# Kernel optimization log

Hardware: AMD Instinct MI355X
Metric: run time of the kernel (lower is better)

Reference implementation:

```python
import jax, jax.numpy as jnp
import numpy as np

N_NODES = 1024
BATCH = 64
N = N_NODES * BATCH          # 65536 total nodes
BBX, LBL = 7, 1
H1, H2, H3 = 512, 16, 4096
LAT = 512
NCLS = 160
N_EDGES = 262144


def setup_inputs() -> dict:
    key = jax.random.key(0)
    ks = jax.random.split(key, 20)
    g = lambda k, shape: (jax.random.normal(k, shape, jnp.float32) * 0.02)
    inp = dict(
        E=jax.random.randint(ks[0], (2, N_EDGES), 0, N, dtype=jnp.int64),
        X_data=jax.random.normal(ks[1], (N, BBX + LBL), jnp.float32),
        class_labels=jax.random.uniform(ks[2], (BATCH * NCLS,), jnp.float32),
        # GCNConv weights (no bias, no normalize, no self-loops)
        W_g1=g(ks[3], (BBX + LBL, H1)),
        W_g2=g(ks[4], (H1, H2)),
        # dense layers ([in, out] convention; y = x @ W + b)
        W_box=g(ks[5], (BBX, H2)), b_box=jnp.zeros((H2,), jnp.float32),
        W_lbl=g(ks[6], (LBL, H2)), b_lbl=jnp.zeros((H2,), jnp.float32),
        W_d1=g(ks[7], (H2 * N_NODES, H3)), b_d1=jnp.zeros((H3,), jnp.float32),
        W_d2=g(ks[8], (H2 * N_NODES + NCLS, H3)), b_d2=jnp.zeros((H3,), jnp.float32),
        W_d3=g(ks[9], (H3, H3)), b_d3=jnp.zeros((H3,), jnp.float32),
        W_z=g(ks[10], (H3, LAT)), b_z=jnp.zeros((LAT,), jnp.float32),
    )
    return inp


def reference(E, X_data, class_labels, W_g1, W_g2, W_box, b_box, W_lbl, b_lbl,
              W_d1, b_d1, W_d2, b_d2, W_d3, b_d3, W_z, b_z):
    relu = jax.nn.relu
    src, dst = E[0], E[1]
    # GCNConv (normalize=False, add_self_loops=False, bias=False):
    # out[i] = sum_{(j->i) in E} (x @ W)[j]
    x = jax.ops.segment_sum((X_data @ W_g1)[src], dst, num_segments=N)   # [N, H1]
    x = jax.ops.segment_sum((x @ W_g2)[src], dst, num_segments=N)        # [N, H2]
    x = x.reshape(BATCH, N_NODES * H2)                                   # [B, 16*num_nodes]
    boxes = relu(X_data[:, 1:].reshape(BATCH, N_NODES, BBX) @ W_box + b_box)
    labels = relu(X_data[:, :1].reshape(BATCH, N_NODES, LBL) @ W_lbl + b_lbl)
    mix = (boxes + labels).reshape(BATCH, N_NODES * H2)
    mix = relu(mix @ W_d1 + b_d1)                                        # [B, H3]
    cls = class_labels.reshape(BATCH, NCLS)
    x = jnp.concatenate([cls, x], axis=-1)                               # [B, NCLS + 16*num_nodes]
    x = relu(x @ W_d2 + b_d2)
    x = x + mix
    x = relu(x @ W_d3 + b_d3)
    x = relu(x @ W_d3 + b_d3)
    z_mean = relu(x @ W_z + b_z)
    z_logvar = relu(x @ W_z + b_z)
    return (z_mean, z_logvar)
```

## Files before the change

### kernel.cpp

```cpp
#include <hip/hip_runtime.h>
#include <stdint.h>

typedef unsigned short u16;
typedef short bf16x8 __attribute__((ext_vector_type(8)));
typedef short bf16x4 __attribute__((ext_vector_type(4)));
typedef float f32x4 __attribute__((ext_vector_type(4)));

#define NTOT   65536
#define NB     64
#define NEDGE  262144
#define H3     4096
#define LATD   512
#define NCLS_  160
#define K1     16384
#define K2     16544

static __device__ __forceinline__ u16 f2b(float f) {
  uint32_t x = __float_as_uint(f);
  return (u16)((x + 0x7FFFu + ((x >> 16) & 1u)) >> 16);
}

__global__ void k_hist(const int* __restrict__ E, int* __restrict__ cnt,
                       const float* __restrict__ Wg1, const float* __restrict__ Wg2,
                       float* __restrict__ Wc) {
  int e = blockIdx.x * 256 + threadIdx.x;
  atomicAdd(&cnt[E[NEDGE + e]], 1);
  if (blockIdx.x == 0 && threadIdx.x < 128) {
    int c = threadIdx.x >> 4, h = threadIdx.x & 15;
    float acc = 0.f;
    for (int k = 0; k < 512; ++k) acc += Wg1[c * 512 + k] * Wg2[k * 16 + h];
    Wc[c * 16 + h] = acc;
  }
}

__global__ __launch_bounds__(1024) void k_scan(const int* __restrict__ cnt,
                                               int* __restrict__ off,
                                               int* __restrict__ cur) {
  __shared__ int wsum[16];
  const int t = threadIdx.x;
  const int lane = t & 63, w = t >> 6;
  const int base = t << 6;
  int s = 0;
  const int4* c4 = (const int4*)(cnt + base);
  #pragma unroll 4
  for (int i = 0; i < 16; ++i) { int4 v = c4[i]; s += v.x + v.y + v.z + v.w; }
  int sc = s;
  #pragma unroll
  for (int d = 1; d < 64; d <<= 1) {
    int u = __shfl_up(sc, d);
    if (lane >= d) sc += u;
  }
  if (lane == 63) wsum[w] = sc;
  __syncthreads();
  if (w == 0 && lane < 16) {
    int v = wsum[lane];
    #pragma unroll
    for (int d = 1; d < 16; d <<= 1) {
      int u = __shfl_up(v, d);
      if (lane >= d) v += u;
    }
    wsum[lane] = v;
  }
  __syncthreads();
  int run = (w == 0 ? 0 : wsum[w - 1]) + (sc - s);
  int4* o4 = (int4*)(off + base);
  int4* u4 = (int4*)(cur + base);
  #pragma unroll 4
  for (int i = 0; i < 16; ++i) {
    int4 v = c4[i];
    int4 r;
    r.x = run; run += v.x;
    r.y = run; run += v.y;
    r.z = run; run += v.z;
    r.w = run; run += v.w;
    o4[i] = r; u4[i] = r;
  }
}

__global__ void k_scatter(const int* __restrict__ E, int* __restrict__ cur,
                          int* __restrict__ csr) {
  int e = blockIdx.x * 256 + threadIdx.x;
  int p = atomicAdd(&cur[E[NEDGE + e]], 1);
  csr[p] = E[e];
}

__global__ void k_gather(const int* __restrict__ off, const int* __restrict__ cnt,
                         const int* __restrict__ csr, const float* __restrict__ In,
                         float* __restrict__ Out) {
  int t = blockIdx.x * 256 + threadIdx.x;
  int n = t >> 3, c = t & 7;
  int b = off[n], e = b + cnt[n];
  float acc = 0.f;
  for (int j = b; j < e; ++j) acc += In[(size_t)csr[j] * 8 + c];
  Out[(size_t)n * 8 + c] = acc;
}

__global__ void k_nodes(const float* __restrict__ S2, const float* __restrict__ Wc,
                        const float* __restrict__ X,
                        const float* __restrict__ Wbox, const float* __restrict__ bbox,
                        const float* __restrict__ Wlbl, const float* __restrict__ blbl,
                        const float* __restrict__ cls,
                        u16* __restrict__ Abuf, u16* __restrict__ Mbuf) {
  int idx = blockIdx.x * 256 + threadIdx.x;
  if (idx < NB * NCLS_) {
    int m = idx / NCLS_, i = idx - m * NCLS_;
    Abuf[(size_t)m * K2 + i] = f2b(cls[idx]);
  }
  if (idx >= NTOT * 16) return;
  int n = idx >> 4, h = idx & 15;
  int m = n >> 10, nl = n & 1023;
  const float* s2 = S2 + (size_t)n * 8;
  float xg = 0.f;
  #pragma unroll
  for (int c = 0; c < 8; ++c) xg += s2[c] * Wc[c * 16 + h];
  Abuf[(size_t)m * K2 + 160 + nl * 16 + h] = f2b(xg);
  const float* xr = X + (size_t)n * 8;
  float box = bbox[h];
  #pragma unroll
  for (int c = 0; c < 7; ++c) box += xr[1 + c] * Wbox[c * 16 + h];
  box = box > 0.f ? box : 0.f;
  float lb = xr[0] * Wlbl[h] + blbl[h];
  lb = lb > 0.f ? lb : 0.f;
  Mbuf[(size_t)m * K1 + nl * 16 + h] = f2b(box + lb);
}

#define CVTPK(dst, lo, hi) \
  asm("v_cvt_pk_bf16_f32 %0, %1, %2" : "=v"(dst) : "v"(lo), "v"(hi))

#define WPACK(I2, WwR)                                                         \
  { const int n_ = (l << 2) + (I2);                                            \
    const int sw_ = ((n_ >> 1) ^ (n_ >> 2)) & 3;                               \
    uint32_t q0, q1, q2, q3;                                                   \
    CVTPK(q0, ws0[I2], ws1[I2]);                                               \
    CVTPK(q1, ws2[I2], ws3[I2]);                                               \
    CVTPK(q2, ws4[I2], ws5[I2]);                                               \
    CVTPK(q3, ws6[I2], ws7[I2]);                                               \
    uint4 pk_ = {q0, q1, q2, q3};                                              \
    *(uint4*)(&WwR[n_ * 32 + ((wv ^ sw_) << 3)]) = pk_; }

#define WLOADS(II)                                                             \
  { const float* gw_ = gW + (size_t)(II) * stepW;                              \
    ws0 = *(const f32x4*)(gw_);                                                \
    ws1 = *(const f32x4*)(gw_ + Nw);                                           \
    ws2 = *(const f32x4*)(gw_ + 2 * Nw);                                       \
    ws3 = *(const f32x4*)(gw_ + 3 * Nw);                                       \
    ws4 = *(const f32x4*)(gw_ + 4 * Nw);                                       \
    ws5 = *(const f32x4*)(gw_ + 5 * Nw);                                       \
    ws6 = *(const f32x4*)(gw_ + 6 * Nw);                                       \
    ws7 = *(const f32x4*)(gw_ + 7 * Nw);                                       \
    aS  = *(const int4*)(gA + (size_t)(II) * 32); }

#define MFMA_BF16 __builtin_amdgcn_mfma_f32_16x16x32_bf16

#define GEMM_STEP(ST, ArD, WrD, AwR, WwR)                                      \
  {                                                                            \
    bf16x8 a0 = *(const bf16x8*)(&ArD[foA]);                                   \
    bf16x8 a1 = *(const bf16x8*)(&ArD[foA + 512]);                             \
    bf16x8 a2 = *(const bf16x8*)(&ArD[foA + 1024]);                            \
    bf16x8 a3 = *(const bf16x8*)(&ArD[foA + 1536]);                            \
    bf16x8 b0 = *(const bf16x8*)(&WrD[foB]);                                   \
    bf16x8 b1 = *(const bf16x8*)(&WrD[foB + 512]);                             \
    bf16x8 b2 = *(const bf16x8*)(&WrD[foB + 1024]);                            \
    bf16x8 b3 = *(const bf16x8*)(&WrD[foB + 1536]);                            \
    *(int4*)(&AwR[t * 8]) = aS;                                                \
    WPACK(0, WwR) WPACK(1, WwR) WPACK(2, WwR) WPACK(3, WwR)                    \
    { const int ii = (ST) + 2 < ns ? (ST) + 2 : ns - 1;                        \
      WLOADS(ii) }                                                             \
    acc00 = MFMA_BF16(a0, b0, acc00, 0, 0, 0);                                 \
    acc01 = MFMA_BF16(a0, b1, acc01, 0, 0, 0);                                 \
    acc02 = MFMA_BF16(a0, b2, acc02, 0, 0, 0);                                 \
    acc03 = MFMA_BF16(a0, b3, acc03, 0, 0, 0);                                 \
    acc10 = MFMA_BF16(a1, b0, acc10, 0, 0, 0);                                 \
    acc11 = MFMA_BF16(a1, b1, acc11, 0, 0, 0);                                 \
    acc12 = MFMA_BF16(a1, b2, acc12, 0, 0, 0);                                 \
    acc13 = MFMA_BF16(a1, b3, acc13, 0, 0, 0);                                 \
    acc20 = MFMA_BF16(a2, b0, acc20, 0, 0, 0);                                 \
    acc21 = MFMA_BF16(a2, b1, acc21, 0, 0, 0);                                 \
    acc22 = MFMA_BF16(a2, b2, acc22, 0, 0, 0);                                 \
    acc23 = MFMA_BF16(a2, b3, acc23, 0, 0, 0);                                 \
    acc30 = MFMA_BF16(a3, b0, acc30, 0, 0, 0);                                 \
    acc31 = MFMA_BF16(a3, b1, acc31, 0, 0, 0);                                 \
    acc32 = MFMA_BF16(a3, b2, acc32, 0, 0, 0);                                 \
    acc33 = MFMA_BF16(a3, b3, acc33, 0, 0, 0);                                 \
    asm volatile("s_waitcnt lgkmcnt(0)" ::: "memory");                         \
    __builtin_amdgcn_s_barrier();                                              \
    asm volatile("" ::: "memory");                                             \
  }

__global__ __launch_bounds__(256) void k_gemm(
    const u16* __restrict__ A0, const u16* __restrict__ A1, int lda0, int lda1,
    const float* __restrict__ W0, const float* __restrict__ W1, int Nw,
    int tot0, int tot1, int per0, int per1, int slabBase1,
    float* __restrict__ Cs)
{
  __shared__ u16 lA0[2048];
  __shared__ u16 lA1[2048];
  __shared__ u16 lW0[8192];
  __shared__ u16 lW1[8192];

  const u16* A; int lda; const float* W; int tot, per, slab;
  if (blockIdx.z == 0) { A = A0; lda = lda0; W = W0; tot = tot0; per = per0; slab = blockIdx.y; }
  else                 { A = A1; lda = lda1; W = W1; tot = tot1; per = per1; slab = slabBase1 + blockIdx.y; }

  const int n0  = blockIdx.x << 8;
  const int sp0 = blockIdx.y * per;
  int ns = tot - sp0; if (ns > per) ns = per;
  if (ns <= 0) return;
  const int t  = threadIdx.x;
  const int l  = t & 63;
  const int wv = t >> 6;

  const int rA  = t >> 2;
  const int cAg = (t & 3) ^ ((rA >> 1) & 3);
  const u16* gA = A + (size_t)rA * lda + cAg * 8 + (size_t)sp0 * 32;

  const float* gW = W + (size_t)(sp0 * 32 + wv * 8) * Nw + n0 + l * 4;
  const size_t stepW = (size_t)32 * Nw;

  const int g4 = l >> 4;
  const int li = l & 15;
  const int foA = li * 32 + ((g4 ^ ((li >> 1) & 3)) << 3);
  const int foB = wv * 2048 + li * 32 +
                  ((g4 ^ (((li >> 1) ^ (li >> 2)) & 3)) << 3);

  f32x4 z4 = {0.f, 0.f, 0.f, 0.f};
  f32x4 acc00 = z4, acc01 = z4, acc02 = z4, acc03 = z4;
  f32x4 acc10 = z4, acc11 = z4, acc12 = z4, acc13 = z4;
  f32x4 acc20 = z4, acc21 = z4, acc22 = z4, acc23 = z4;
  f32x4 acc30 = z4, acc31 = z4, acc32 = z4, acc33 = z4;

  f32x4 ws0, ws1, ws2, ws3, ws4, ws5, ws6, ws7;
  int4 aS;

  WLOADS(0)
  *(int4*)(&lA0[t * 8]) = aS;
  WPACK(0, lW0) WPACK(1, lW0) WPACK(2, lW0) WPACK(3, lW0)
  { const int i1 = 1 < ns ? 1 : 0;
    WLOADS(i1) }
  asm volatile("s_waitcnt lgkmcnt(0)" ::: "memory");
  __builtin_amdgcn_s_barrier();
  asm volatile("" ::: "memory");

  int st = 0;
  for (; st + 2 <= ns; st += 2) {
    GEMM_STEP(st,     lA0, lW0, lA1, lW1)
    GEMM_STEP(st + 1, lA1, lW1, lA0, lW0)
  }
  if (st < ns) {
    GEMM_STEP(st, lA0, lW0, lA1, lW1)
  }

  float* base = Cs + (size_t)slab * NB * Nw + n0 + wv * 64 + li;
  #pragma unroll
  for (int j = 0; j < 4; ++j) {
    float* r0 = base + (size_t)(g4 * 4 + j) * Nw;
    r0[0]                    = acc00[j];
    r0[16]                   = acc01[j];
    r0[32]                   = acc02[j];
    r0[48]                   = acc03[j];
    float* r1 = r0 + 16 * Nw;
    r1[0]                    = acc10[j];
    r1[16]                   = acc11[j];
    r1[32]                   = acc12[j];
    r1[48]                   = acc13[j];
    float* r2 = r0 + 32 * Nw;
    r2[0]                    = acc20[j];
    r2[16]                   = acc21[j];
    r2[32]                   = acc22[j];
    r2[48]                   = acc23[j];
    float* r3 = r0 + 48 * Nw;
    r3[0]                    = acc30[j];
    r3[16]                   = acc31[j];
    r3[32]                   = acc32[j];
    r3[48]                   = acc33[j];
  }
}

__global__ void k_ep12(const float* __restrict__ Cs,
                       const float* __restrict__ b1, const float* __restrict__ b2,
                       u16* __restrict__ A3) {
  int i = blockIdx.x * 256 + threadIdx.x;
  if (i >= NB * H3) return;
  float mix = b1[i & (H3 - 1)];
  float v   = b2[i & (H3 - 1)];
  #pragma unroll 4
  for (int s = 0; s < 16; ++s)  mix += Cs[(size_t)s * (NB * H3) + i];
  #pragma unroll 4
  for (int s = 16; s < 32; ++s) v   += Cs[(size_t)s * (NB * H3) + i];
  mix = mix > 0.f ? mix : 0.f;
  v   = v   > 0.f ? v   : 0.f;
  A3[i] = f2b(v + mix);
}

__global__ void k_ep(const float* __restrict__ Cs, int nslab, int slabElems,
                     const float* __restrict__ bias, u16* __restrict__ outb,
                     int colmask, int total) {
  int i = blockIdx.x * 256 + threadIdx.x;
  if (i >= total) return;
  float v = bias[i & colmask];
  #pragma unroll 4
  for (int s = 0; s < nslab; ++s) v += Cs[(size_t)s * slabElems + i];
  v = v > 0.f ? v : 0.f;
  outb[i] = f2b(v);
}

__global__ void k_ep5(const float* __restrict__ Cs, int nslab,
                      const float* __restrict__ bz, float* __restrict__ out) {
  int i = blockIdx.x * 256 + threadIdx.x;
  if (i >= NB * LATD) return;
  float v = bz[i & 511];
  #pragma unroll 4
  for (int s = 0; s < nslab; ++s) v += Cs[(size_t)s * (NB * LATD) + i];
  v = v > 0.f ? v : 0.f;
  out[i] = v;
  out[NB * LATD + i] = v;
}

extern "C" void kernel_launch(void* const* d_in, const int* in_sizes, int n_in,
                              void* d_out, int out_size, void* d_ws, size_t ws_size,
                              hipStream_t stream) {
  const int*   E    = (const int*)d_in[0];
  const float* X    = (const float*)d_in[1];
  const float* cls  = (const float*)d_in[2];
  const float* Wg1  = (const float*)d_in[3];
  const float* Wg2  = (const float*)d_in[4];
  const float* Wbox = (const float*)d_in[5];
  const float* bbox = (const float*)d_in[6];
  const float* Wlbl = (const float*)d_in[7];
  const float* blbl = (const float*)d_in[8];
  const float* Wd1  = (const float*)d_in[9];
  const float* bd1  = (const float*)d_in[10];
  const float* Wd2  = (const float*)d_in[11];
  const float* bd2  = (const float*)d_in[12];
  const float* Wd3  = (const float*)d_in[13];
  const float* bd3  = (const float*)d_in[14];
  const float* Wz   = (const float*)d_in[15];
  const float* bz   = (const float*)d_in[16];

  char* ws = (char*)d_ws;
  int*   cnt  = (int*)  (ws + 0x000000);
  int*   off  = (int*)  (ws + 0x040000);
  int*   cur  = (int*)  (ws + 0x080000);
  int*   csr  = (int*)  (ws + 0x0C0000);
  float* S1   = (float*)(ws + 0x1C0000);
  float* S2   = (float*)(ws + 0x3C0000);
  float* Wc   = (float*)(ws + 0x5C0000);
  u16*   A3   = (u16*)  (ws + 0x5C1000);
  u16*   A4   = (u16*)  (ws + 0x641000);
  u16*   A5   = (u16*)  (ws + 0x6C1000);
  u16*   Mbuf = (u16*)  (ws + 0x741000);
  u16*   Abuf = (u16*)  (ws + 0x941000);
  float* Cslb = (float*)(ws + 0xB50000);

  hipMemsetAsync(cnt, 0, 0x40000, stream);
  k_hist   <<<NEDGE / 256, 256, 0, stream>>>(E, cnt, Wg1, Wg2, Wc);
  k_scan   <<<1, 1024, 0, stream>>>(cnt, off, cur);
  k_scatter<<<NEDGE / 256, 256, 0, stream>>>(E, cur, csr);
  k_gather <<<NTOT * 8 / 256, 256, 0, stream>>>(off, cnt, csr, X,  S1);
  k_gather <<<NTOT * 8 / 256, 256, 0, stream>>>(off, cnt, csr, S1, S2);
  k_nodes  <<<NTOT * 16 / 256, 256, 0, stream>>>(S2, Wc, X, Wbox, bbox, Wlbl, blbl,
                                                 cls, Abuf, Mbuf);

  { dim3 g(16, 16, 2);
    k_gemm<<<g, 256, 0, stream>>>(Mbuf, Abuf, K1, K2, Wd1, Wd2, H3,
                                  512, 517, 32, 33, 16, Cslb); }
  k_ep12<<<NB * H3 / 256, 256, 0, stream>>>(Cslb, bd1, bd2, A3);

  { dim3 g(16, 16, 1);
    k_gemm<<<g, 256, 0, stream>>>(A3, A3, H3, H3, Wd3, Wd3, H3,
                                  128, 128, 8, 8, 0, Cslb); }
  k_ep<<<NB * H3 / 256, 256, 0, stream>>>(Cslb, 16, NB * H3, bd3, A4, H3 - 1, NB * H3);

  { dim3 g(16, 16, 1);
    k_gemm<<<g, 256, 0, stream>>>(A4, A4, H3, H3, Wd3, Wd3, H3,
                                  128, 128, 8, 8, 0, Cslb); }
  k_ep<<<NB * H3 / 256, 256, 0, stream>>>(Cslb, 16, NB * H3, bd3, A5, H3 - 1, NB * H3);

  { dim3 g(2, 32, 1);
    k_gemm<<<g, 256, 0, stream>>>(A5, A5, H3, H3, Wz, Wz, LATD,
                                  128, 128, 4, 4, 0, Cslb); }
  k_ep5<<<NB * LATD / 256, 256, 0, stream>>>(Cslb, 32, bz, (float*)d_out);
}
```

Measured before the change: 296.7 us.

## Make GEMM weight tiles wave-private, load A to registers, double split-K

Each wave of the GEMM now stages only its own 64-column slice of the weight tile in LDS. This removes the block-wide barrier at every K step. The A operand is loaded straight from global memory into registers, one step ahead, instead of going through shared memory. Split-K slabs are doubled (grid y 16→32, per-slab steps halved) to put more blocks in flight on the bandwidth-bound weight stream, and launch bounds now ask for 3 blocks per CU. In exchange, each wave issues redundant A global loads and more fp32 partial-sum slabs are written and then reduced in the epilogues.

```diff
diff --git a/kernel.cpp b/kernel.cpp
--- a/kernel.cpp
+++ b/kernel.cpp
@@ -127,16 +127,7 @@
 #define CVTPK(dst, lo, hi) \
   asm("v_cvt_pk_bf16_f32 %0, %1, %2" : "=v"(dst) : "v"(lo), "v"(hi))
 
-#define WPACK(I2, WwR)                                                         \
-  { const int n_ = (l << 2) + (I2);                                            \
-    const int sw_ = ((n_ >> 1) ^ (n_ >> 2)) & 3;                               \
-    uint32_t q0, q1, q2, q3;                                                   \
-    CVTPK(q0, ws0[I2], ws1[I2]);                                               \
-    CVTPK(q1, ws2[I2], ws3[I2]);                                               \
-    CVTPK(q2, ws4[I2], ws5[I2]);                                               \
-    CVTPK(q3, ws6[I2], ws7[I2]);                                               \
-    uint4 pk_ = {q0, q1, q2, q3};                                              \
-    *(uint4*)(&WwR[n_ * 32 + ((wv ^ sw_) << 3)]) = pk_; }
+#define MFMA_BF16 __builtin_amdgcn_mfma_f32_16x16x32_bf16
 
 #define WLOADS(II)                                                             \
   { const float* gw_ = gW + (size_t)(II) * stepW;                              \
@@ -147,25 +138,33 @@
     ws4 = *(const f32x4*)(gw_ + 4 * Nw);                                       \
     ws5 = *(const f32x4*)(gw_ + 5 * Nw);                                       \
     ws6 = *(const f32x4*)(gw_ + 6 * Nw);                                       \
-    ws7 = *(const f32x4*)(gw_ + 7 * Nw);                                       \
-    aS  = *(const int4*)(gA + (size_t)(II) * 32); }
-
-#define MFMA_BF16 __builtin_amdgcn_mfma_f32_16x16x32_bf16
-
-#define GEMM_STEP(ST, ArD, WrD, AwR, WwR)                                      \
+    ws7 = *(const f32x4*)(gw_ + 7 * Nw); }
+
+#define ALOADS(II)                                                             \
+  { const u16* ga_ = gA + (size_t)(II) * 32;                                   \
+    a0 = *(const bf16x8*)(ga_);                                                \
+    a1 = *(const bf16x8*)(ga_ + rtA);                                          \
+    a2 = *(const bf16x8*)(ga_ + 2 * rtA);                                      \
+    a3 = *(const bf16x8*)(ga_ + 3 * rtA); }
+
+#define WPACK(I2, Lw)                                                          \
+  { uint32_t q0, q1, q2, q3;                                                   \
+    CVTPK(q0, ws0[I2], ws1[I2]);                                               \
+    CVTPK(q1, ws2[I2], ws3[I2]);                                               \
+    CVTPK(q2, ws4[I2], ws5[I2]);                                               \
+    CVTPK(q3, ws6[I2], ws7[I2]);                                               \
+    uint4 pk_ = {q0, q1, q2, q3};                                              \
+    *(uint4*)(&Lw[wo##I2]) = pk_; }
+
+#define GEMM_STEP(ST, Lr, Lw)                                                  \
   {                                                                            \
-    bf16x8 a0 = *(const bf16x8*)(&ArD[foA]);                                   \
-    bf16x8 a1 = *(const bf16x8*)(&ArD[foA + 512]);                             \
-    bf16x8 a2 = *(const bf16x8*)(&ArD[foA + 1024]);                            \
-    bf16x8 a3 = *(const bf16x8*)(&ArD[foA + 1536]);                            \
-    bf16x8 b0 = *(const bf16x8*)(&WrD[foB]);                                   \
-    bf16x8 b1 = *(const bf16x8*)(&WrD[foB + 512]);                             \
-    bf16x8 b2 = *(const bf16x8*)(&WrD[foB + 1024]);                            \
-    bf16x8 b3 = *(const bf16x8*)(&WrD[foB + 1536]);                            \
-    *(int4*)(&AwR[t * 8]) = aS;                                                \
-    WPACK(0, WwR) WPACK(1, WwR) WPACK(2, WwR) WPACK(3, WwR)                    \
-    { const int ii = (ST) + 2 < ns ? (ST) + 2 : ns - 1;                        \
-      WLOADS(ii) }                                                             \
+    bf16x8 b0 = *(const bf16x8*)(&Lr[ro]);                                     \
+    bf16x8 b1 = *(const bf16x8*)(&Lr[ro + 512]);                               \
+    bf16x8 b2 = *(const bf16x8*)(&Lr[ro + 1024]);                              \
+    bf16x8 b3 = *(const bf16x8*)(&Lr[ro + 1536]);                              \
+    WPACK(0, Lw) WPACK(1, Lw) WPACK(2, Lw) WPACK(3, Lw)                        \
+    { const int i2_ = (ST) + 2 < ns ? (ST) + 2 : ns - 1;                       \
+      WLOADS(i2_) }                                                            \
     acc00 = MFMA_BF16(a0, b0, acc00, 0, 0, 0);                                 \
     acc01 = MFMA_BF16(a0, b1, acc01, 0, 0, 0);                                 \
     acc02 = MFMA_BF16(a0, b2, acc02, 0, 0, 0);                                 \
@@ -182,21 +181,19 @@
     acc31 = MFMA_BF16(a3, b1, acc31, 0, 0, 0);                                 \
     acc32 = MFMA_BF16(a3, b2, acc32, 0, 0, 0);                                 \
     acc33 = MFMA_BF16(a3, b3, acc33, 0, 0, 0);                                 \
+    { const int i1_ = (ST) + 1 < ns ? (ST) + 1 : ns - 1;                       \
+      ALOADS(i1_) }                                                            \
     asm volatile("s_waitcnt lgkmcnt(0)" ::: "memory");                         \
-    __builtin_amdgcn_s_barrier();                                              \
-    asm volatile("" ::: "memory");                                             \
-  }
-
-__global__ __launch_bounds__(256) void k_gemm(
+  }
+
+__global__ __launch_bounds__(256, 3) void k_gemm(
     const u16* __restrict__ A0, const u16* __restrict__ A1, int lda0, int lda1,
     const float* __restrict__ W0, const float* __restrict__ W1, int Nw,
     int tot0, int tot1, int per0, int per1, int slabBase1,
     float* __restrict__ Cs)
 {
-  __shared__ u16 lA0[2048];
-  __shared__ u16 lA1[2048];
-  __shared__ u16 lW0[8192];
-  __shared__ u16 lW1[8192];
+  __shared__ u16 lWb0[8192];
+  __shared__ u16 lWb1[8192];
 
   const u16* A; int lda; const float* W; int tot, per, slab;
   if (blockIdx.z == 0) { A = A0; lda = lda0; W = W0; tot = tot0; per = per0; slab = blockIdx.y; }
@@ -209,19 +206,22 @@
   const int t  = threadIdx.x;
   const int l  = t & 63;
   const int wv = t >> 6;
-
-  const int rA  = t >> 2;
-  const int cAg = (t & 3) ^ ((rA >> 1) & 3);
-  const u16* gA = A + (size_t)rA * lda + cAg * 8 + (size_t)sp0 * 32;
-
-  const float* gW = W + (size_t)(sp0 * 32 + wv * 8) * Nw + n0 + l * 4;
-  const size_t stepW = (size_t)32 * Nw;
-
   const int g4 = l >> 4;
   const int li = l & 15;
-  const int foA = li * 32 + ((g4 ^ ((li >> 1) & 3)) << 3);
-  const int foB = wv * 2048 + li * 32 +
-                  ((g4 ^ (((li >> 1) ^ (li >> 2)) & 3)) << 3);
+  const int wvbase = wv << 11;
+
+  const float* gW = W + (size_t)(sp0 * 32 + g4 * 8) * Nw + n0 + wv * 64 + 4 * li;
+  const size_t stepW = (size_t)32 * Nw;
+
+  const u16* gA = A + (size_t)li * lda + (size_t)sp0 * 32 + g4 * 8;
+  const size_t rtA = (size_t)16 * lda;
+
+  #define WOFFc(nn) (wvbase + (nn) * 32 + (((g4 ^ (((nn) >> 1) ^ ((nn) >> 2))) & 3) << 3))
+  const int wo0 = WOFFc(4 * li + 0);
+  const int wo1 = WOFFc(4 * li + 1);
+  const int wo2 = WOFFc(4 * li + 2);
+  const int wo3 = WOFFc(4 * li + 3);
+  const int ro  = wvbase + li * 32 + (((g4 ^ ((li >> 1) ^ (li >> 2))) & 3) << 3);
 
   f32x4 z4 = {0.f, 0.f, 0.f, 0.f};
   f32x4 acc00 = z4, acc01 = z4, acc02 = z4, acc03 = z4;
@@ -230,49 +230,47 @@
   f32x4 acc30 = z4, acc31 = z4, acc32 = z4, acc33 = z4;
 
   f32x4 ws0, ws1, ws2, ws3, ws4, ws5, ws6, ws7;
-  int4 aS;
+  bf16x8 a0, a1, a2, a3;
 
   WLOADS(0)
-  *(int4*)(&lA0[t * 8]) = aS;
-  WPACK(0, lW0) WPACK(1, lW0) WPACK(2, lW0) WPACK(3, lW0)
-  { const int i1 = 1 < ns ? 1 : 0;
-    WLOADS(i1) }
+  ALOADS(0)
+  WPACK(0, lWb0) WPACK(1, lWb0) WPACK(2, lWb0) WPACK(3, lWb0)
+  { const int i1_ = 1 < ns ? 1 : 0;
+    WLOADS(i1_) }
   asm volatile("s_waitcnt lgkmcnt(0)" ::: "memory");
-  __builtin_amdgcn_s_barrier();
-  asm volatile("" ::: "memory");
 
   int st = 0;
   for (; st + 2 <= ns; st += 2) {
-    GEMM_STEP(st,     lA0, lW0, lA1, lW1)
-    GEMM_STEP(st + 1, lA1, lW1, lA0, lW0)
+    GEMM_STEP(st,     lWb0, lWb1)
+    GEMM_STEP(st + 1, lWb1, lWb0)
   }
   if (st < ns) {
-    GEMM_STEP(st, lA0, lW0, lA1, lW1)
+    GEMM_STEP(st, lWb0, lWb1)
   }
 
   float* base = Cs + (size_t)slab * NB * Nw + n0 + wv * 64 + li;
   #pragma unroll
   for (int j = 0; j < 4; ++j) {
     float* r0 = base + (size_t)(g4 * 4 + j) * Nw;
-    r0[0]                    = acc00[j];
-    r0[16]                   = acc01[j];
-    r0[32]                   = acc02[j];
-    r0[48]                   = acc03[j];
+    r0[0]  = acc00[j];
+    r0[16] = acc01[j];
+    r0[32] = acc02[j];
+    r0[48] = acc03[j];
     float* r1 = r0 + 16 * Nw;
-    r1[0]                    = acc10[j];
-    r1[16]                   = acc11[j];
-    r1[32]                   = acc12[j];
-    r1[48]                   = acc13[j];
+    r1[0]  = acc10[j];
+    r1[16] = acc11[j];
+    r1[32] = acc12[j];
+    r1[48] = acc13[j];
     float* r2 = r0 + 32 * Nw;
-    r2[0]                    = acc20[j];
-    r2[16]                   = acc21[j];
-    r2[32]                   = acc22[j];
-    r2[48]                   = acc23[j];
+    r2[0]  = acc20[j];
+    r2[16] = acc21[j];
+    r2[32] = acc22[j];
+    r2[48] = acc23[j];
     float* r3 = r0 + 48 * Nw;
-    r3[0]                    = acc30[j];
-    r3[16]                   = acc31[j];
-    r3[32]                   = acc32[j];
-    r3[48]                   = acc33[j];
+    r3[0]  = acc30[j];
+    r3[16] = acc31[j];
+    r3[32] = acc32[j];
+    r3[48] = acc33[j];
   }
 }
 
@@ -284,9 +282,9 @@
   float mix = b1[i & (H3 - 1)];
   float v   = b2[i & (H3 - 1)];
   #pragma unroll 4
-  for (int s = 0; s < 16; ++s)  mix += Cs[(size_t)s * (NB * H3) + i];
-  #pragma unroll 4
-  for (int s = 16; s < 32; ++s) v   += Cs[(size_t)s * (NB * H3) + i];
+  for (int s = 0; s < 32; ++s)  mix += Cs[(size_t)s * (NB * H3) + i];
+  #pragma unroll 4
+  for (int s = 32; s < 63; ++s) v   += Cs[(size_t)s * (NB * H3) + i];
   mix = mix > 0.f ? mix : 0.f;
   v   = v   > 0.f ? v   : 0.f;
   A3[i] = f2b(v + mix);
@@ -361,20 +359,20 @@
   k_nodes  <<<NTOT * 16 / 256, 256, 0, stream>>>(S2, Wc, X, Wbox, bbox, Wlbl, blbl,
                                                  cls, Abuf, Mbuf);
 
-  { dim3 g(16, 16, 2);
+  { dim3 g(16, 32, 2);
     k_gemm<<<g, 256, 0, stream>>>(Mbuf, Abuf, K1, K2, Wd1, Wd2, H3,
-                                  512, 517, 32, 33, 16, Cslb); }
+                                  512, 517, 16, 17, 32, Cslb); }
   k_ep12<<<NB * H3 / 256, 256, 0, stream>>>(Cslb, bd1, bd2, A3);
 
-  { dim3 g(16, 16, 1);
+  { dim3 g(16, 32, 1);
     k_gemm<<<g, 256, 0, stream>>>(A3, A3, H3, H3, Wd3, Wd3, H3,
-                                  128, 128, 8, 8, 0, Cslb); }
-  k_ep<<<NB * H3 / 256, 256, 0, stream>>>(Cslb, 16, NB * H3, bd3, A4, H3 - 1, NB * H3);
-
-  { dim3 g(16, 16, 1);
+                                  128, 128, 4, 4, 0, Cslb); }
+  k_ep<<<NB * H3 / 256, 256, 0, stream>>>(Cslb, 32, NB * H3, bd3, A4, H3 - 1, NB * H3);
+
+  { dim3 g(16, 32, 1);
     k_gemm<<<g, 256, 0, stream>>>(A4, A4, H3, H3, Wd3, Wd3, H3,
-                                  128, 128, 8, 8, 0, Cslb); }
-  k_ep<<<NB * H3 / 256, 256, 0, stream>>>(Cslb, 16, NB * H3, bd3, A5, H3 - 1, NB * H3);
+                                  128, 128, 4, 4, 0, Cslb); }
+  k_ep<<<NB * H3 / 256, 256, 0, stream>>>(Cslb, 32, NB * H3, bd3, A5, H3 - 1, NB * H3);
 
   { dim3 g(2, 32, 1);
     k_gemm<<<g, 256, 0, stream>>>(A5, A5, H3, H3, Wz, Wz, LATD,
```

Result: slower. 370.5 us (+24.8%).

## Replace split-K GEMMs for dense-3 and z layers with fused full-K kernel

Applied to the files above, without the earlier changes.

Adds a k_gemm2 kernel for the two W_d3 layers and the W_z layer. Each block covers all 64 rows and a 32-column strip over the full K, with bias and ReLU applied in the epilogue. This removes the split-K partial-sum slabs and the separate reduction kernels, cutting launches and fp32 scratch traffic. The cost is far fewer blocks (128 and 16) and a shallow two-step prefetch, so weight streaming may become latency-bound and leave much of the GPU idle.

```diff
diff --git a/kernel.cpp b/kernel.cpp
--- a/kernel.cpp
+++ b/kernel.cpp
@@ -127,6 +127,8 @@
 #define CVTPK(dst, lo, hi) \
   asm("v_cvt_pk_bf16_f32 %0, %1, %2" : "=v"(dst) : "v"(lo), "v"(hi))
 
+#define MFMA_BF16 __builtin_amdgcn_mfma_f32_16x16x32_bf16
+
 #define WPACK(I2, WwR)                                                         \
   { const int n_ = (l << 2) + (I2);                                            \
     const int sw_ = ((n_ >> 1) ^ (n_ >> 2)) & 3;                               \
@@ -149,8 +151,6 @@
     ws6 = *(const f32x4*)(gw_ + 6 * Nw);                                       \
     ws7 = *(const f32x4*)(gw_ + 7 * Nw);                                       \
     aS  = *(const int4*)(gA + (size_t)(II) * 32); }
-
-#define MFMA_BF16 __builtin_amdgcn_mfma_f32_16x16x32_bf16
 
 #define GEMM_STEP(ST, ArD, WrD, AwR, WwR)                                      \
   {                                                                            \
@@ -254,25 +254,123 @@
   #pragma unroll
   for (int j = 0; j < 4; ++j) {
     float* r0 = base + (size_t)(g4 * 4 + j) * Nw;
-    r0[0]                    = acc00[j];
-    r0[16]                   = acc01[j];
-    r0[32]                   = acc02[j];
-    r0[48]                   = acc03[j];
+    r0[0]  = acc00[j];
+    r0[16] = acc01[j];
+    r0[32] = acc02[j];
+    r0[48] = acc03[j];
     float* r1 = r0 + 16 * Nw;
-    r1[0]                    = acc10[j];
-    r1[16]                   = acc11[j];
-    r1[32]                   = acc12[j];
-    r1[48]                   = acc13[j];
+    r1[0]  = acc10[j];
+    r1[16] = acc11[j];
+    r1[32] = acc12[j];
+    r1[48] = acc13[j];
     float* r2 = r0 + 32 * Nw;
-    r2[0]                    = acc20[j];
-    r2[16]                   = acc21[j];
-    r2[32]                   = acc22[j];
-    r2[48]                   = acc23[j];
+    r2[0]  = acc20[j];
+    r2[16] = acc21[j];
+    r2[32] = acc22[j];
+    r2[48] = acc23[j];
     float* r3 = r0 + 48 * Nw;
-    r3[0]                    = acc30[j];
-    r3[16]                   = acc31[j];
-    r3[32]                   = acc32[j];
-    r3[48]                   = acc33[j];
+    r3[0]  = acc30[j];
+    r3[16] = acc31[j];
+    r3[32] = acc32[j];
+    r3[48] = acc33[j];
+  }
+}
+
+#define WLOADS2(II)                                                            \
+  { const float* gw_ = gW2 + (size_t)(II) * stepW2;                            \
+    vs0 = *(const f32x4*)(gw_);                                                \
+    vs1 = *(const f32x4*)(gw_ + Nw);                                           \
+    vs2 = *(const f32x4*)(gw_ + 2 * Nw);                                       \
+    vs3 = *(const f32x4*)(gw_ + 3 * Nw);                                       \
+    aS2 = *(const bf16x8*)(gA2 + (size_t)(II) * 32); }
+
+#define WPACK2(C_, Lw)                                                         \
+  { uint32_t q0, q1;                                                           \
+    CVTPK(q0, vs0[C_], vs1[C_]);                                               \
+    CVTPK(q1, vs2[C_], vs3[C_]);                                               \
+    uint2 pk_ = {q0, q1};                                                      \
+    *(uint2*)(&Lw[wo2_##C_]) = pk_; }
+
+#define GEMM2_STEP(ST, Lr, Lw)                                                 \
+  {                                                                            \
+    bf16x8 b0 = *(const bf16x8*)(&Lr[ro2]);                                    \
+    bf16x8 b1 = *(const bf16x8*)(&Lr[ro2 + 512]);                              \
+    bf16x8 a  = aC;                                                            \
+    WPACK2(0, Lw) WPACK2(1, Lw) WPACK2(2, Lw) WPACK2(3, Lw)                    \
+    { const int ii = (ST) + 2 < 128 ? (ST) + 2 : 127;                          \
+      aC = aS2;                                                                \
+      WLOADS2(ii) }                                                            \
+    acc0 = MFMA_BF16(a, b0, acc0, 0, 0, 0);                                    \
+    acc1 = MFMA_BF16(a, b1, acc1, 0, 0, 0);                                    \
+    asm volatile("s_waitcnt lgkmcnt(0)" ::: "memory");                         \
+  }
+
+template<int WRITEF>
+__global__ __launch_bounds__(256) void k_gemm2(
+    const u16* __restrict__ A, const float* __restrict__ W, int Nw,
+    const float* __restrict__ bias, u16* __restrict__ outb,
+    float* __restrict__ outf)
+{
+  __shared__ u16 lB0[4096];
+  __shared__ u16 lB1[4096];
+  const int t  = threadIdx.x;
+  const int l  = t & 63;
+  const int wv = t >> 6;
+  const int g4 = l >> 4;
+  const int li = l & 15;
+  const int n0 = blockIdx.x << 5;
+  const int wvb = wv << 10;
+
+  const float* gW2 = W + (size_t)(4 * (l >> 3)) * Nw + n0 + (l & 7) * 4;
+  const size_t stepW2 = (size_t)32 * Nw;
+  const u16* gA2 = A + (size_t)(wv * 16 + li) * 4096 + g4 * 8;
+
+  const int kc_  = (l >> 3) >> 1;
+  const int klo_ = ((l >> 3) & 1) << 2;
+  #define WO2(C_) (wvb + ((l & 7) * 4 + (C_)) * 32 +                           \
+    ((kc_ ^ ((((((l & 7) * 4 + (C_)) >> 1) ^ (((l & 7) * 4 + (C_)) >> 2))) & 3)) << 3) + klo_)
+  const int wo2_0 = WO2(0);
+  const int wo2_1 = WO2(1);
+  const int wo2_2 = WO2(2);
+  const int wo2_3 = WO2(3);
+  const int ro2 = wvb + li * 32 + ((g4 ^ (((li >> 1) ^ (li >> 2)) & 3)) << 3);
+
+  f32x4 z4 = {0.f, 0.f, 0.f, 0.f};
+  f32x4 acc0 = z4, acc1 = z4;
+  f32x4 vs0, vs1, vs2, vs3;
+  bf16x8 aS2, aC;
+
+  WLOADS2(0)
+  aC = aS2;
+  WPACK2(0, lB0) WPACK2(1, lB0) WPACK2(2, lB0) WPACK2(3, lB0)
+  WLOADS2(1)
+  asm volatile("s_waitcnt lgkmcnt(0)" ::: "memory");
+
+  for (int st = 0; st < 128; st += 2) {
+    GEMM2_STEP(st,     lB0, lB1)
+    GEMM2_STEP(st + 1, lB1, lB0)
+  }
+
+  const float b0v = bias[n0 + li];
+  const float b1v = bias[n0 + 16 + li];
+  #pragma unroll
+  for (int j = 0; j < 4; ++j) {
+    const int R = wv * 16 + g4 * 4 + j;
+    float v0 = acc0[j] + b0v;
+    float v1 = acc1[j] + b1v;
+    v0 = v0 > 0.f ? v0 : 0.f;
+    v1 = v1 > 0.f ? v1 : 0.f;
+    if (WRITEF) {
+      float* p = outf + (size_t)R * Nw + n0 + li;
+      p[0]  = v0;
+      p[16] = v1;
+      p[NB * LATD]      = v0;
+      p[NB * LATD + 16] = v1;
+    } else {
+      u16* p = outb + (size_t)R * Nw + n0 + li;
+      p[0]  = f2b(v0);
+      p[16] = f2b(v1);
+    }
   }
 }
 
@@ -290,30 +388,6 @@
   mix = mix > 0.f ? mix : 0.f;
   v   = v   > 0.f ? v   : 0.f;
   A3[i] = f2b(v + mix);
-}
-
-__global__ void k_ep(const float* __restrict__ Cs, int nslab, int slabElems,
-                     const float* __restrict__ bias, u16* __restrict__ outb,
-                     int colmask, int total) {
-  int i = blockIdx.x * 256 + threadIdx.x;
-  if (i >= total) return;
-  float v = bias[i & colmask];
-  #pragma unroll 4
-  for (int s = 0; s < nslab; ++s) v += Cs[(size_t)s * slabElems + i];
-  v = v > 0.f ? v : 0.f;
-  outb[i] = f2b(v);
-}
-
-__global__ void k_ep5(const float* __restrict__ Cs, int nslab,
-                      const float* __restrict__ bz, float* __restrict__ out) {
-  int i = blockIdx.x * 256 + threadIdx.x;
-  if (i >= NB * LATD) return;
-  float v = bz[i & 511];
-  #pragma unroll 4
-  for (int s = 0; s < nslab; ++s) v += Cs[(size_t)s * (NB * LATD) + i];
-  v = v > 0.f ? v : 0.f;
-  out[i] = v;
-  out[NB * LATD + i] = v;
 }
 
 extern "C" void kernel_launch(void* const* d_in, const int* in_sizes, int n_in,
@@ -366,18 +440,8 @@
                                   512, 517, 32, 33, 16, Cslb); }
   k_ep12<<<NB * H3 / 256, 256, 0, stream>>>(Cslb, bd1, bd2, A3);
 
-  { dim3 g(16, 16, 1);
-    k_gemm<<<g, 256, 0, stream>>>(A3, A3, H3, H3, Wd3, Wd3, H3,
-                                  128, 128, 8, 8, 0, Cslb); }
-  k_ep<<<NB * H3 / 256, 256, 0, stream>>>(Cslb, 16, NB * H3, bd3, A4, H3 - 1, NB * H3);
-
-  { dim3 g(16, 16, 1);
-    k_gemm<<<g, 256, 0, stream>>>(A4, A4, H3, H3, Wd3, Wd3, H3,
-                                  128, 128, 8, 8, 0, Cslb); }
-  k_ep<<<NB * H3 / 256, 256, 0, stream>>>(Cslb, 16, NB * H3, bd3, A5, H3 - 1, NB * H3);
-
-  { dim3 g(2, 32, 1);
-    k_gemm<<<g, 256, 0, stream>>>(A5, A5, H3, H3, Wz, Wz, LATD,
-                                  128, 128, 4, 4, 0, Cslb); }
-  k_ep5<<<NB * LATD / 256, 256, 0, stream>>>(Cslb, 32, bz, (float*)d_out);
-}
+  k_gemm2<0><<<H3 / 32, 256, 0, stream>>>(A3, Wd3, H3, bd3, A4, nullptr);
+  k_gemm2<0><<<H3 / 32, 256, 0, stream>>>(A4, Wd3, H3, bd3, A5, nullptr);
+  k_gemm2<1><<<LATD / 32, 256, 0, stream>>>(A5, Wz, LATD, bz, nullptr,
+                                            (float*)d_out);
+}
```

After: 399.1 us. +34.5%, slower.
